# Optimization experiments

Measured on AMD Instinct MI355X. Metric: run time of the kernel, lower is better.

Reference implementation:

```python
import jax, jax.numpy as jnp
import numpy as np

B, T, V, C, H, E, O, NL = 2048, 128, 256, 32, 128, 256, 256, 3
BN = E // 8  # bottleneck = 32
G = 3 * H    # stacked gate dim (r,z,n) = 384
LN_EPS = 1e-5


def setup_inputs() -> dict:
    key = jax.random.key(0)
    ks = jax.random.split(key, 19)
    s = 0.1
    return {
        "tokens": jax.random.randint(ks[0], (B, T), 0, V),
        "lang_ids": jax.random.randint(ks[1], (B,), 0, NL),
        "char_embed": jax.random.normal(ks[2], (V, C)) * s,
        "w_ih_f": jax.random.normal(ks[3], (G, C)) * s,
        "w_hh_f": jax.random.normal(ks[4], (G, H)) * s,
        "b_ih_f": jax.random.normal(ks[5], (G,)) * s,
        "b_hh_f": jax.random.normal(ks[6], (G,)) * s,
        "w_ih_b": jax.random.normal(ks[7], (G, C)) * s,
        "w_hh_b": jax.random.normal(ks[8], (G, H)) * s,
        "b_ih_b": jax.random.normal(ks[9], (G,)) * s,
        "b_hh_b": jax.random.normal(ks[10], (G,)) * s,
        "down_w": jax.random.normal(ks[11], (NL, BN, E)) * s,
        "down_b": jax.random.normal(ks[12], (NL, BN)) * s,
        "up_w": jax.random.normal(ks[13], (NL, E, BN)) * s,
        "up_b": jax.random.normal(ks[14], (NL, E)) * s,
        "ln_g": jnp.ones((NL, E)),
        "ln_b": jnp.zeros((NL, E)),
        "proj_w": jax.random.normal(ks[15], (O, E)) * s,
        "proj_b": jax.random.normal(ks[16], (O,)) * s,
    }


def _gru_last_hidden(x, w_ih, w_hh, b_ih, b_hh):
    """x: [B,T,C] -> final hidden [B,H]. torch GRU gate order (r,z,n)."""
    xp = jnp.einsum('btc,gc->btg', x, w_ih) + b_ih        # [B,T,3H]
    xp = jnp.swapaxes(xp, 0, 1)                           # [T,B,3H]
    h0 = jnp.zeros((x.shape[0], w_hh.shape[1]), x.dtype)

    def step(h, xp_t):
        gh = h @ w_hh.T + b_hh
        xr, xz, xn = jnp.split(xp_t, 3, axis=-1)
        hr, hz, hn = jnp.split(gh, 3, axis=-1)
        r = jax.nn.sigmoid(xr + hr)
        z = jax.nn.sigmoid(xz + hz)
        n = jnp.tanh(xn + r * hn)
        return (1.0 - z) * n + z * h, None

    hT, _ = jax.lax.scan(step, h0, xp)
    return hT


def reference(tokens, lang_ids, char_embed,
              w_ih_f, w_hh_f, b_ih_f, b_hh_f,
              w_ih_b, w_hh_b, b_ih_b, b_hh_b,
              down_w, down_b, up_w, up_b, ln_g, ln_b,
              proj_w, proj_b):
    emb = char_embed[tokens]                              # [B,T,C]
    h_f = _gru_last_hidden(emb, w_ih_f, w_hh_f, b_ih_f, b_hh_f)
    h_b = _gru_last_hidden(emb[:, ::-1], w_ih_b, w_hh_b, b_ih_b, b_hh_b)
    feat = jnp.concatenate([h_f, h_b], axis=-1)           # [B,E]

    # per-sample language-routed bottleneck adapter (gathered expert params)
    hid = jax.nn.gelu(
        jnp.einsum('be,bde->bd', feat, down_w[lang_ids]) + down_b[lang_ids],
        approximate=False)                                # [B,BN]
    adapted = jnp.einsum('bd,bed->be', hid, up_w[lang_ids]) + up_b[lang_ids]
    x = feat + adapted
    mu = jnp.mean(x, axis=-1, keepdims=True)
    var = jnp.var(x, axis=-1, keepdims=True)
    xn = (x - mu) / jnp.sqrt(var + LN_EPS)
    y = xn * ln_g[lang_ids] + ln_b[lang_ids]              # [B,E]

    return y @ proj_w.T + proj_b                          # [B,O]
```

## Files before the change

### kernel.cpp

```cpp
#include <hip/hip_runtime.h>
#include <hip/hip_bf16.h>
#include <hip/hip_fp16.h>

#define Bn 2048
#define Tn 128
#define Vn 256
#define Cn 32
#define Hn 128
#define En 256
#define On 256
#define Gn 384
#define BNn 32

typedef _Float16 f16;
typedef __attribute__((ext_vector_type(8))) _Float16 h8;
typedef __attribute__((ext_vector_type(4))) _Float16 h4;
typedef __attribute__((ext_vector_type(2))) _Float16 h2;
typedef __attribute__((ext_vector_type(2))) __fp16 hb2;
typedef __attribute__((ext_vector_type(4))) float f4;

#define LOG2E 1.4426950408889634f

__device__ __forceinline__ f16 hexp2(f16 x) {
  f16 r;
  asm("v_exp_f16 %0, %1" : "=v"(r) : "v"(x));
  return r;
}
__device__ __forceinline__ f16 hrcp(f16 x) {
  f16 r;
  asm("v_rcp_f16 %0, %1" : "=v"(r) : "v"(x));
  return r;
}
__device__ __forceinline__ h2 pkrtz(float a, float b) {
  return __builtin_bit_cast(h2, __builtin_amdgcn_cvt_pkrtz(a, b));
}
__device__ __forceinline__ float dot2(h2 a, h2 b, float c) {
#if __has_builtin(__builtin_amdgcn_fdot2)
  return __builtin_amdgcn_fdot2(__builtin_bit_cast(hb2, a), __builtin_bit_cast(hb2, b), c, false);
#else
  return fmaf((float)a[0], (float)b[0], fmaf((float)a[1], (float)b[1], c));
#endif
}

__global__ void build_table_k(const float* __restrict__ emb,
                              const float* __restrict__ wf,
                              const float* __restrict__ bif,
                              const float* __restrict__ bhf,
                              const float* __restrict__ wb,
                              const float* __restrict__ bib,
                              const float* __restrict__ bhb,
                              f16* __restrict__ xt) {
  const int dir = blockIdx.x >> 8;
  const int v = blockIdx.x & 255;
  const int j = threadIdx.x;
  const float* w = dir ? wb : wf;
  const float* bi = dir ? bib : bif;
  const float* bh = dir ? bhb : bhf;
  const float sc[3] = {-LOG2E, -LOG2E, 2.0f * LOG2E};
  h4 o;
  o[3] = (f16)0.f;
#pragma unroll
  for (int ga = 0; ga < 3; ++ga) {
    const int g = ga * Hn + j;
    float acc = bi[g] + (ga < 2 ? bh[g] : 0.f);
    const f4* wr = (const f4*)(w + g * Cn);
    const f4* er = (const f4*)(emb + v * Cn);
#pragma unroll
    for (int q = 0; q < 8; ++q) {
      f4 wv = wr[q], ev = er[q];
      acc = fmaf(ev.x, wv.x, acc);
      acc = fmaf(ev.y, wv.y, acc);
      acc = fmaf(ev.z, wv.z, acc);
      acc = fmaf(ev.w, wv.w, acc);
    }
    o[ga] = (f16)(acc * sc[ga]);
  }
  *(h4*)&xt[((dir * Vn + v) * Hn + j) * 4] = o;
}

__global__ void cvt_k(const float* __restrict__ pw,
                      const float* __restrict__ dw,
                      const float* __restrict__ uw,
                      f16* __restrict__ pwh,
                      f16* __restrict__ dwh,
                      f16* __restrict__ uwh) {
  const int i = blockIdx.x * 256 + threadIdx.x;
  pwh[i] = (f16)pw[i];
  if (i < 3 * BNn * En) {
    dwh[i] = (f16)dw[i];
    uwh[i] = (f16)uw[i];
  }
}

__launch_bounds__(512, 2)
__global__ void gru_k(const int* __restrict__ tokens,
                      const float* __restrict__ whhf,
                      const float* __restrict__ bhhf,
                      const float* __restrict__ whhb,
                      const float* __restrict__ bhhb,
                      const f16* __restrict__ xt,
                      float* __restrict__ feat) {
  const int dir = blockIdx.x & 1;
  const int b0 = (blockIdx.x >> 1) * 16;
  const int tid = threadIdx.x;
  const int wv = tid >> 6;
  const int ln = tid & 63;
  const int lr = ln & 15;
  const int lg = ln >> 4;
  const int j = wv * 16 + lr;

  __shared__ f16 hfrag[2 * 2048];
  __shared__ int tokT[Tn * 16];

  for (int i = tid; i < Tn * 16; i += 512) {
    const int t = i >> 4, s = i & 15;
    tokT[i] = tokens[(b0 + s) * Tn + (dir ? (Tn - 1 - t) : t)] << 10;
  }
  for (int i = tid; i < 2 * 2048; i += 512) hfrag[i] = (f16)0.f;

  const float* whh = dir ? whhb : whhf;
  const float* bhh = dir ? bhhb : bhhf;
  const char* tab = (const char*)(xt + dir * (Vn * Hn * 4));

  const float gsc[3] = {-LOG2E, -LOG2E, 2.0f * LOG2E};
  h8 Bf[3][4];
#pragma unroll
  for (int ga = 0; ga < 3; ++ga) {
    const float* wr = whh + (ga * Hn + j) * Hn + lg * 8;
#pragma unroll
    for (int kk = 0; kk < 4; ++kk) {
      h8 b;
#pragma unroll
      for (int i = 0; i < 8; ++i) b[i] = (f16)(wr[kk * 32 + i] * gsc[ga]);
      Bf[ga][kk] = b;
    }
  }
  const float b2 = bhh[2 * Hn + j] * (2.0f * LOG2E);
  const f4 BH2 = {b2, b2, b2, b2};
  const f4 Z4 = {0.f, 0.f, 0.f, 0.f};

  __syncthreads();

  const int aadr = (lg * 256 + lr * 16) ^ ((lg & 1) << 5);
  int wadr[4];
  {
    const int wmask = ((j >> 3) & 1) << 5;
    const int wbase = (j >> 3) * 256 + (j & 7) * 2 + lg * 64;
#pragma unroll
    for (int r = 0; r < 4; ++r) wadr[r] = (wbase + r * 16) ^ wmask;
  }
  const int tadr = lg * 16;
  const int jb = j * 8;

  int4 tkA = *(const int4*)((const char*)tokT + tadr);
  h4 xc0, xc1, xc2, xc3, xn0, xn1, xn2, xn3;
  xc0 = *(const h4*)(tab + tkA.x + jb);
  xc1 = *(const h4*)(tab + tkA.y + jb);
  xc2 = *(const h4*)(tab + tkA.z + jb);
  xc3 = *(const h4*)(tab + tkA.w + jb);
  int4 tkB = *(const int4*)((const char*)tokT + 64 + tadr);

  f16 h0 = (f16)0.f, h1 = (f16)0.f, h2v = (f16)0.f, h3 = (f16)0.f;
  const f16 ONE = (f16)1.f;
  const f16 TWO = (f16)2.f;

#define GATE(HV, CV, I, ANH)                                                   \
  {                                                                            \
    h2 arz = pkrtz(aR[I], aZ[I]);                                              \
    h2 srz = {CV[0], CV[1]};                                                   \
    h2 t = srz + arz;                                                          \
    h2 e = {hexp2(t[0]), hexp2(t[1])};                                         \
    h2 d = e + (h2){ONE, ONE};                                                 \
    const f16 rg = hrcp(d[0]);                                                 \
    const f16 zg = hrcp(d[1]);                                                 \
    const f16 ng = ONE - TWO * hrcp(ONE + hexp2(rg * ANH + CV[2]));            \
    HV = zg * (HV - ng) + ng;                                                  \
    *(f16*)(hw + wadr[I]) = HV;                                                \
  }

#define GRU_BODY(T, P, C0, C1, C2, C3, N0, N1, N2, N3, TKc, TKn)               \
  {                                                                            \
    const char* hb = (const char*)hfrag + (P) * 4096;                          \
    h8 A0 = *(const h8*)(hb + aadr + 0 * 1024);                                \
    h8 A1 = *(const h8*)(hb + aadr + 1 * 1024);                                \
    h8 A2 = *(const h8*)(hb + aadr + 2 * 1024);                                \
    h8 A3 = *(const h8*)(hb + aadr + 3 * 1024);                                \
    N0 = *(const h4*)(tab + TKc.x + jb);                                       \
    N1 = *(const h4*)(tab + TKc.y + jb);                                       \
    N2 = *(const h4*)(tab + TKc.z + jb);                                       \
    N3 = *(const h4*)(tab + TKc.w + jb);                                       \
    {                                                                          \
      const int tt = ((T) + 2 < Tn) ? ((T) + 2) : (Tn - 1);                    \
      TKn = *(const int4*)((const char*)tokT + tt * 64 + tadr);                \
    }                                                                          \
    f4 aR = __builtin_amdgcn_mfma_f32_16x16x32_f16(A0, Bf[0][0], Z4, 0, 0, 0); \
    f4 aZ = __builtin_amdgcn_mfma_f32_16x16x32_f16(A0, Bf[1][0], Z4, 0, 0, 0); \
    f4 aN = __builtin_amdgcn_mfma_f32_16x16x32_f16(A0, Bf[2][0], BH2, 0, 0, 0);\
    aR = __builtin_amdgcn_mfma_f32_16x16x32_f16(A1, Bf[0][1], aR, 0, 0, 0);    \
    aZ = __builtin_amdgcn_mfma_f32_16x16x32_f16(A1, Bf[1][1], aZ, 0, 0, 0);    \
    aN = __builtin_amdgcn_mfma_f32_16x16x32_f16(A1, Bf[2][1], aN, 0, 0, 0);    \
    aR = __builtin_amdgcn_mfma_f32_16x16x32_f16(A2, Bf[0][2], aR, 0, 0, 0);    \
    aZ = __builtin_amdgcn_mfma_f32_16x16x32_f16(A2, Bf[1][2], aZ, 0, 0, 0);    \
    aN = __builtin_amdgcn_mfma_f32_16x16x32_f16(A2, Bf[2][2], aN, 0, 0, 0);    \
    aR = __builtin_amdgcn_mfma_f32_16x16x32_f16(A3, Bf[0][3], aR, 0, 0, 0);    \
    aZ = __builtin_amdgcn_mfma_f32_16x16x32_f16(A3, Bf[1][3], aZ, 0, 0, 0);    \
    aN = __builtin_amdgcn_mfma_f32_16x16x32_f16(A3, Bf[2][3], aN, 0, 0, 0);    \
    char* hw = (char*)hfrag + ((P) ^ 1) * 4096;                                \
    h2 an01 = pkrtz(aN[0], aN[1]);                                             \
    h2 an23 = pkrtz(aN[2], aN[3]);                                             \
    GATE(h0, C0, 0, an01[0])                                                   \
    GATE(h1, C1, 1, an01[1])                                                   \
    GATE(h2v, C2, 2, an23[0])                                                  \
    GATE(h3, C3, 3, an23[1])                                                   \
    asm volatile("s_waitcnt lgkmcnt(0)\n\ts_barrier" ::: "memory");            \
  }

#pragma unroll 1
  for (int t = 0; t < Tn; t += 2) {
    GRU_BODY(t, 0, xc0, xc1, xc2, xc3, xn0, xn1, xn2, xn3, tkB, tkA)
    GRU_BODY(t + 1, 1, xn0, xn1, xn2, xn3, xc0, xc1, xc2, xc3, tkA, tkB)
  }
#undef GRU_BODY
#undef GATE

  feat[(b0 + lg * 4 + 0) * En + dir * Hn + j] = (float)h0;
  feat[(b0 + lg * 4 + 1) * En + dir * Hn + j] = (float)h1;
  feat[(b0 + lg * 4 + 2) * En + dir * Hn + j] = (float)h2v;
  feat[(b0 + lg * 4 + 3) * En + dir * Hn + j] = (float)h3;
}

__launch_bounds__(256, 2)
__global__ void epi_k(const float* __restrict__ feat,
                      const int* __restrict__ lang_ids,
                      const f16* __restrict__ dwh,
                      const float* __restrict__ down_b,
                      const f16* __restrict__ uwh,
                      const float* __restrict__ up_b,
                      const float* __restrict__ ln_g,
                      const float* __restrict__ ln_b,
                      const f16* __restrict__ pwh,
                      const float* __restrict__ proj_b,
                      float* __restrict__ out) {
  const int tid = threadIdx.x;
  const int wv = tid >> 6, ln = tid & 63;
  const int b0 = blockIdx.x * 8;

  __shared__ f16 fl16[8][En];
  __shared__ f16 yA[16][En + 8];

#pragma unroll
  for (int s = 0; s < 8; ++s) fl16[s][tid] = (f16)feat[(b0 + s) * En + tid];
  __syncthreads();

#pragma unroll 1
  for (int si = 0; si < 2; ++si) {
    const int s = wv * 2 + si;
    const int lang = lang_ids[b0 + s];

    const int d = ln & 31, hf = ln >> 5;
    const h8* dw8 = (const h8*)(dwh + (lang * BNn + d) * En + hf * 128);
    const h8* fs8 = (const h8*)&fl16[s][hf * 128];
    float pacc = 0.f;
#pragma unroll
    for (int q = 0; q < 16; ++q) {
      h8 a = fs8[q], w = dw8[q];
#pragma unroll
      for (int p = 0; p < 4; ++p)
        pacc = dot2((h2){a[2 * p], a[2 * p + 1]}, (h2){w[2 * p], w[2 * p + 1]}, pacc);
    }
    pacc += __shfl_xor(pacc, 32);
    const float hv = pacc + down_b[lang * BNn + d];
    const float hid = 0.5f * hv * (1.0f + erff(hv * 0.70710678118f));

    h2 hp[16];
#pragma unroll
    for (int p = 0; p < 16; ++p)
      hp[p] = pkrtz(__shfl(hid, 2 * p), __shfl(hid, 2 * p + 1));

    const int e0 = ln * 4;
    float x[4];
    float s1 = 0.f, s2 = 0.f;
#pragma unroll
    for (int i = 0; i < 4; ++i) {
      const h8* uw8 = (const h8*)(uwh + (lang * En + e0 + i) * BNn);
      float a = 0.f;
#pragma unroll
      for (int q = 0; q < 4; ++q) {
        h8 u = uw8[q];
#pragma unroll
        for (int p = 0; p < 4; ++p)
          a = dot2(hp[4 * q + p], (h2){u[2 * p], u[2 * p + 1]}, a);
      }
      x[i] = a + (float)fl16[s][e0 + i] + up_b[lang * En + e0 + i];
      s1 += x[i];
      s2 = fmaf(x[i], x[i], s2);
    }
#pragma unroll
    for (int off = 32; off >= 1; off >>= 1) {
      s1 += __shfl_xor(s1, off);
      s2 += __shfl_xor(s2, off);
    }
    const float mu = s1 * (1.0f / En);
    const float var = s2 * (1.0f / En) - mu * mu;
    const float rs = rsqrtf(var + 1e-5f);
#pragma unroll
    for (int i = 0; i < 4; ++i) {
      const float yv = (x[i] - mu) * rs * ln_g[lang * En + e0 + i] + ln_b[lang * En + e0 + i];
      yA[s][e0 + i] = (f16)yv;
    }
  }
  __syncthreads();

  const int lr = ln & 15, lg = ln >> 4;
  f4 acc[4];
#pragma unroll
  for (int tt = 0; tt < 4; ++tt) {
    const float pb = proj_b[wv * 64 + tt * 16 + lr];
    acc[tt] = (f4){pb, pb, pb, pb};
  }
#pragma unroll
  for (int kk = 0; kk < 8; ++kk) {
    h8 aF = *(const h8*)(&yA[lr][kk * 32 + lg * 8]);
#pragma unroll
    for (int tt = 0; tt < 4; ++tt) {
      const int o0 = wv * 64 + tt * 16;
      h8 bF = *(const h8*)(pwh + (o0 + lr) * En + kk * 32 + lg * 8);
      acc[tt] = __builtin_amdgcn_mfma_f32_16x16x32_f16(aF, bF, acc[tt], 0, 0, 0);
    }
  }
  if (lg < 2) {
#pragma unroll
    for (int tt = 0; tt < 4; ++tt) {
      const int o0 = wv * 64 + tt * 16;
#pragma unroll
      for (int r = 0; r < 4; ++r)
        out[(b0 + lg * 4 + r) * On + o0 + lr] = acc[tt][r];
    }
  }
}

extern "C" void kernel_launch(void* const* d_in, const int* in_sizes, int n_in,
                              void* d_out, int out_size, void* d_ws, size_t ws_size,
                              hipStream_t stream) {
  const int* tokens = (const int*)d_in[0];
  const int* lang_ids = (const int*)d_in[1];
  const float* emb = (const float*)d_in[2];
  const float* w_ih_f = (const float*)d_in[3];
  const float* w_hh_f = (const float*)d_in[4];
  const float* b_ih_f = (const float*)d_in[5];
  const float* b_hh_f = (const float*)d_in[6];
  const float* w_ih_b = (const float*)d_in[7];
  const float* w_hh_b = (const float*)d_in[8];
  const float* b_ih_b = (const float*)d_in[9];
  const float* b_hh_b = (const float*)d_in[10];
  const float* down_w = (const float*)d_in[11];
  const float* down_b = (const float*)d_in[12];
  const float* up_w = (const float*)d_in[13];
  const float* up_b = (const float*)d_in[14];
  const float* ln_g = (const float*)d_in[15];
  const float* ln_b = (const float*)d_in[16];
  const float* proj_w = (const float*)d_in[17];
  const float* proj_b = (const float*)d_in[18];

  char* ws = (char*)d_ws;
  f16* xt = (f16*)ws;
  float* feat = (float*)(ws + 524288);
  f16* pwh = (f16*)(ws + 2621440);
  f16* dwh = (f16*)(ws + 2752512);
  f16* uwh = (f16*)(ws + 2801664);

  build_table_k<<<dim3(512), dim3(128), 0, stream>>>(emb, w_ih_f, b_ih_f, b_hh_f,
                                                     w_ih_b, b_ih_b, b_hh_b, xt);
  cvt_k<<<dim3(256), dim3(256), 0, stream>>>(proj_w, down_w, up_w, pwh, dwh, uwh);
  gru_k<<<dim3(256), dim3(512), 0, stream>>>(tokens, w_hh_f, b_hh_f, w_hh_b, b_hh_b, xt, feat);
  epi_k<<<dim3(256), dim3(256), 0, stream>>>(feat, lang_ids, dwh, down_b, uwh, up_b,
                                             ln_g, ln_b, pwh, proj_b, (float*)d_out);
}
```

Before: 120.5 us.

## Split GRU gate work across two wave halves and vectorize weight conversion

```diff
diff --git a/kernel.cpp b/kernel.cpp
--- a/kernel.cpp
+++ b/kernel.cpp
@@ -84,15 +84,25 @@
                       f16* __restrict__ pwh,
                       f16* __restrict__ dwh,
                       f16* __restrict__ uwh) {
-  const int i = blockIdx.x * 256 + threadIdx.x;
-  pwh[i] = (f16)pw[i];
-  if (i < 3 * BNn * En) {
-    dwh[i] = (f16)dw[i];
-    uwh[i] = (f16)uw[i];
-  }
-}
-
-__launch_bounds__(512, 2)
+  const int i = (blockIdx.x * 256 + threadIdx.x) * 4;
+  if (i < 65536) {
+    f4 v = *(const f4*)(pw + i);
+    h4 o = {(f16)v.x, (f16)v.y, (f16)v.z, (f16)v.w};
+    *(h4*)(pwh + i) = o;
+  } else {
+    const int k = i - 65536;
+    if (k < 3 * BNn * En) {
+      f4 v = *(const f4*)(dw + k);
+      h4 o = {(f16)v.x, (f16)v.y, (f16)v.z, (f16)v.w};
+      *(h4*)(dwh + k) = o;
+      f4 u = *(const f4*)(uw + k);
+      h4 p = {(f16)u.x, (f16)u.y, (f16)u.z, (f16)u.w};
+      *(h4*)(uwh + k) = p;
+    }
+  }
+}
+
+__launch_bounds__(1024, 1)
 __global__ void gru_k(const int* __restrict__ tokens,
                       const float* __restrict__ whhf,
                       const float* __restrict__ bhhf,
@@ -103,7 +113,9 @@
   const int dir = blockIdx.x & 1;
   const int b0 = (blockIdx.x >> 1) * 16;
   const int tid = threadIdx.x;
-  const int wv = tid >> 6;
+  const int wave = tid >> 6;
+  const int hf = wave >> 3;
+  const int wv = wave & 7;
   const int ln = tid & 63;
   const int lr = ln & 15;
   const int lg = ln >> 4;
@@ -112,11 +124,11 @@
   __shared__ f16 hfrag[2 * 2048];
   __shared__ int tokT[Tn * 16];
 
-  for (int i = tid; i < Tn * 16; i += 512) {
+  for (int i = tid; i < Tn * 16; i += 1024) {
     const int t = i >> 4, s = i & 15;
     tokT[i] = tokens[(b0 + s) * Tn + (dir ? (Tn - 1 - t) : t)] << 10;
   }
-  for (int i = tid; i < 2 * 2048; i += 512) hfrag[i] = (f16)0.f;
+  for (int i = tid; i < 2 * 2048; i += 1024) hfrag[i] = (f16)0.f;
 
   const float* whh = dir ? whhb : whhf;
   const float* bhh = dir ? bhhb : bhhf;
@@ -142,31 +154,26 @@
   __syncthreads();
 
   const int aadr = (lg * 256 + lr * 16) ^ ((lg & 1) << 5);
-  int wadr[4];
-  {
-    const int wmask = ((j >> 3) & 1) << 5;
-    const int wbase = (j >> 3) * 256 + (j & 7) * 2 + lg * 64;
-#pragma unroll
-    for (int r = 0; r < 4; ++r) wadr[r] = (wbase + r * 16) ^ wmask;
-  }
-  const int tadr = lg * 16;
+  const int wmask = ((j >> 3) & 1) << 5;
+  const int wbase = (j >> 3) * 256 + (j & 7) * 2 + lg * 64;
+  const int wadr0 = (wbase + (2 * hf + 0) * 16) ^ wmask;
+  const int wadr1 = (wbase + (2 * hf + 1) * 16) ^ wmask;
+  const int tadr = lg * 16 + hf * 8;
   const int jb = j * 8;
 
-  int4 tkA = *(const int4*)((const char*)tokT + tadr);
-  h4 xc0, xc1, xc2, xc3, xn0, xn1, xn2, xn3;
+  int2 tkA = *(const int2*)((const char*)tokT + tadr);
+  h4 xc0, xc1, xn0, xn1;
   xc0 = *(const h4*)(tab + tkA.x + jb);
   xc1 = *(const h4*)(tab + tkA.y + jb);
-  xc2 = *(const h4*)(tab + tkA.z + jb);
-  xc3 = *(const h4*)(tab + tkA.w + jb);
-  int4 tkB = *(const int4*)((const char*)tokT + 64 + tadr);
-
-  f16 h0 = (f16)0.f, h1 = (f16)0.f, h2v = (f16)0.f, h3 = (f16)0.f;
+  int2 tkB = *(const int2*)((const char*)tokT + 64 + tadr);
+
+  f16 h0 = (f16)0.f, h1 = (f16)0.f;
   const f16 ONE = (f16)1.f;
   const f16 TWO = (f16)2.f;
 
-#define GATE(HV, CV, I, ANH)                                                   \
+#define GATE(HV, CV, WA, ARv, AZv, ANH)                                        \
   {                                                                            \
-    h2 arz = pkrtz(aR[I], aZ[I]);                                              \
+    h2 arz = pkrtz(ARv, AZv);                                                  \
     h2 srz = {CV[0], CV[1]};                                                   \
     h2 t = srz + arz;                                                          \
     h2 e = {hexp2(t[0]), hexp2(t[1])};                                         \
@@ -175,10 +182,10 @@
     const f16 zg = hrcp(d[1]);                                                 \
     const f16 ng = ONE - TWO * hrcp(ONE + hexp2(rg * ANH + CV[2]));            \
     HV = zg * (HV - ng) + ng;                                                  \
-    *(f16*)(hw + wadr[I]) = HV;                                                \
-  }
-
-#define GRU_BODY(T, P, C0, C1, C2, C3, N0, N1, N2, N3, TKc, TKn)               \
+    *(f16*)(hw + WA) = HV;                                                     \
+  }
+
+#define GRU_BODY(T, P, C0, C1, N0, N1, TKc, TKn)                               \
   {                                                                            \
     const char* hb = (const char*)hfrag + (P) * 4096;                          \
     h8 A0 = *(const h8*)(hb + aadr + 0 * 1024);                                \
@@ -187,11 +194,9 @@
     h8 A3 = *(const h8*)(hb + aadr + 3 * 1024);                                \
     N0 = *(const h4*)(tab + TKc.x + jb);                                       \
     N1 = *(const h4*)(tab + TKc.y + jb);                                       \
-    N2 = *(const h4*)(tab + TKc.z + jb);                                       \
-    N3 = *(const h4*)(tab + TKc.w + jb);                                       \
     {                                                                          \
       const int tt = ((T) + 2 < Tn) ? ((T) + 2) : (Tn - 1);                    \
-      TKn = *(const int4*)((const char*)tokT + tt * 64 + tadr);                \
+      TKn = *(const int2*)((const char*)tokT + tt * 64 + tadr);                \
     }                                                                          \
     f4 aR = __builtin_amdgcn_mfma_f32_16x16x32_f16(A0, Bf[0][0], Z4, 0, 0, 0); \
     f4 aZ = __builtin_amdgcn_mfma_f32_16x16x32_f16(A0, Bf[1][0], Z4, 0, 0, 0); \
@@ -206,27 +211,28 @@
     aZ = __builtin_amdgcn_mfma_f32_16x16x32_f16(A3, Bf[1][3], aZ, 0, 0, 0);    \
     aN = __builtin_amdgcn_mfma_f32_16x16x32_f16(A3, Bf[2][3], aN, 0, 0, 0);    \
     char* hw = (char*)hfrag + ((P) ^ 1) * 4096;                                \
-    h2 an01 = pkrtz(aN[0], aN[1]);                                             \
-    h2 an23 = pkrtz(aN[2], aN[3]);                                             \
-    GATE(h0, C0, 0, an01[0])                                                   \
-    GATE(h1, C1, 1, an01[1])                                                   \
-    GATE(h2v, C2, 2, an23[0])                                                  \
-    GATE(h3, C3, 3, an23[1])                                                   \
+    if (hf) {                                                                  \
+      h2 an = pkrtz(aN[2], aN[3]);                                             \
+      GATE(h0, C0, wadr0, aR[2], aZ[2], an[0])                                 \
+      GATE(h1, C1, wadr1, aR[3], aZ[3], an[1])                                 \
+    } else {                                                                   \
+      h2 an = pkrtz(aN[0], aN[1]);                                             \
+      GATE(h0, C0, wadr0, aR[0], aZ[0], an[0])                                 \
+      GATE(h1, C1, wadr1, aR[1], aZ[1], an[1])                                 \
+    }                                                                          \
     asm volatile("s_waitcnt lgkmcnt(0)\n\ts_barrier" ::: "memory");            \
   }
 
 #pragma unroll 1
   for (int t = 0; t < Tn; t += 2) {
-    GRU_BODY(t, 0, xc0, xc1, xc2, xc3, xn0, xn1, xn2, xn3, tkB, tkA)
-    GRU_BODY(t + 1, 1, xn0, xn1, xn2, xn3, xc0, xc1, xc2, xc3, tkA, tkB)
+    GRU_BODY(t, 0, xc0, xc1, xn0, xn1, tkB, tkA)
+    GRU_BODY(t + 1, 1, xn0, xn1, xc0, xc1, tkA, tkB)
   }
 #undef GRU_BODY
 #undef GATE
 
-  feat[(b0 + lg * 4 + 0) * En + dir * Hn + j] = (float)h0;
-  feat[(b0 + lg * 4 + 1) * En + dir * Hn + j] = (float)h1;
-  feat[(b0 + lg * 4 + 2) * En + dir * Hn + j] = (float)h2v;
-  feat[(b0 + lg * 4 + 3) * En + dir * Hn + j] = (float)h3;
+  feat[(b0 + lg * 4 + 2 * hf + 0) * En + dir * Hn + j] = (float)h0;
+  feat[(b0 + lg * 4 + 2 * hf + 1) * En + dir * Hn + j] = (float)h1;
 }
 
 __launch_bounds__(256, 2)
@@ -371,8 +377,8 @@
 
   build_table_k<<<dim3(512), dim3(128), 0, stream>>>(emb, w_ih_f, b_ih_f, b_hh_f,
                                                      w_ih_b, b_ih_b, b_hh_b, xt);
-  cvt_k<<<dim3(256), dim3(256), 0, stream>>>(proj_w, down_w, up_w, pwh, dwh, uwh);
-  gru_k<<<dim3(256), dim3(512), 0, stream>>>(tokens, w_hh_f, b_hh_f, w_hh_b, b_hh_b, xt, feat);
+  cvt_k<<<dim3(112), dim3(256), 0, stream>>>(proj_w, down_w, up_w, pwh, dwh, uwh);
+  gru_k<<<dim3(256), dim3(1024), 0, stream>>>(tokens, w_hh_f, b_hh_f, w_hh_b, b_hh_b, xt, feat);
   epi_k<<<dim3(256), dim3(256), 0, stream>>>(feat, lang_ids, dwh, down_b, uwh, up_b,
                                              ln_g, ln_b, pwh, proj_b, (float*)d_out);
 }
```

Result: slower. 141.5 us (+17.4%).
